# Performance work log

Hardware: AMD Instinct MI355X
Metric: run time of the kernel (lower is better)

Reference implementation:

```python
import jax, jax.numpy as jnp
import numpy as np

N = 50000        # node_num
E = 1600000      # num edges
F_IN = 8
HID = 1000
R = 100          # robustness_length


def setup_inputs() -> dict:
    key = jax.random.key(0)
    ks = jax.random.split(key, 16)
    X = jax.random.normal(ks[0], (N, F_IN), dtype=jnp.float32)
    edge_index = jax.random.randint(ks[1], (2, E), 0, N, dtype=jnp.int64)
    s = 1.0 / np.sqrt(F_IN)
    # SAGEConv mean-aggr params (PyG: out = lin_l(aggr) + lin_r(x), lin_r has no bias)
    lin_l_w = jax.random.uniform(ks[2], (1, F_IN), jnp.float32, -s, s)
    lin_l_b = jax.random.uniform(ks[3], (1,), jnp.float32, -s, s)
    lin_r_w = jax.random.uniform(ks[4], (1, F_IN), jnp.float32, -s, s)
    # SAGEConv max-aggr params
    lin_l1_w = jax.random.uniform(ks[5], (1, F_IN), jnp.float32, -s, s)
    lin_l1_b = jax.random.uniform(ks[6], (1,), jnp.float32, -s, s)
    lin_r1_w = jax.random.uniform(ks[7], (1, F_IN), jnp.float32, -s, s)
    # MLP params
    s0 = 1.0 / np.sqrt(N)
    W0 = jax.random.uniform(ks[8], (HID, N), jnp.float32, -s0, s0)
    b0 = jax.random.uniform(ks[9], (HID,), jnp.float32, -s0, s0)
    s1 = 1.0 / np.sqrt(HID)
    W1 = jax.random.uniform(ks[10], (HID, HID), jnp.float32, -s1, s1)
    b1 = jax.random.uniform(ks[11], (HID,), jnp.float32, -s1, s1)
    W2 = jax.random.uniform(ks[12], (R, HID), jnp.float32, -s1, s1)
    b2 = jax.random.uniform(ks[13], (R,), jnp.float32, -s1, s1)
    return dict(X=X, edge_index=edge_index,
                lin_l_w=lin_l_w, lin_l_b=lin_l_b, lin_r_w=lin_r_w,
                lin_l1_w=lin_l1_w, lin_l1_b=lin_l1_b, lin_r1_w=lin_r1_w,
                W0=W0, b0=b0, W1=W1, b1=b1, W2=W2, b2=b2)


def reference(X, edge_index, lin_l_w, lin_l_b, lin_r_w,
              lin_l1_w, lin_l1_b, lin_r1_w,
              W0, b0, W1, b1, W2, b2):
    src, dst = edge_index[0], edge_index[1]
    msgs = X[src]  # [E, F_IN] gathered neighbor features
    cnt = jax.ops.segment_sum(jnp.ones((E,), jnp.float32), dst, num_segments=N)
    # mean aggregation (empty -> 0)
    agg_mean = jax.ops.segment_sum(msgs, dst, num_segments=N) / jnp.maximum(cnt, 1.0)[:, None]
    # max aggregation (empty -> 0, per PyG scatter-max fill)
    agg_max = jax.ops.segment_max(msgs, dst, num_segments=N)
    agg_max = jnp.where(cnt[:, None] > 0, agg_max, 0.0)
    # SAGEConv: lin_l(aggr) + lin_r(x)
    h_mean = jax.nn.relu(agg_mean @ lin_l_w.T + lin_l_b + X @ lin_r_w.T)   # [N,1]
    h_max = jax.nn.relu(agg_max @ lin_l1_w.T + lin_l1_b + X @ lin_r1_w.T)  # [N,1]
    x = (h_mean + h_max).reshape(-1)  # [N]
    X_embedding = x
    h = jax.nn.relu(W0 @ x + b0)
    h = jax.nn.relu(W1 @ h + b1)
    out = jax.nn.relu(W2 @ h + b2)
    return (X_embedding, out)
```

## Files before the change

### kernel.cpp

```cpp
#include <hip/hip_runtime.h>

#define N_NODES 50000
#define N_EDGES 1600000
#define F_IN 8
#define HID 1000
#define R_OUT 100

#define NGRP 8
#define BSHIFT 6
#define NPB 64
#define NB 782
#define CAP_B 448
#define NCHUNK0 25


__device__ __forceinline__ unsigned fkey(float f) {
    unsigned b = __float_as_uint(f);
    return (b & 0x80000000u) ? ~b : (b | 0x80000000u);
}
__device__ __forceinline__ float funkey(unsigned k) {
    unsigned b = (k & 0x80000000u) ? (k & 0x7fffffffu) : ~k;
    return __uint_as_float(b);
}

__global__ void init_ws(unsigned* __restrict__ p, int n) {
    int i = blockIdx.x * blockDim.x + threadIdx.x;
    if (i < n) p[i] = 0u;
}

__global__ void bin_kernel(const int* __restrict__ ei,
                           const float* __restrict__ X,
                           const float* __restrict__ wl,
                           int* __restrict__ bcnt,
                           unsigned* __restrict__ binned,
                           int* __restrict__ ovf_cnt,
                           float* __restrict__ ovf_sum,
                           unsigned* __restrict__ ovf_max) {
    int e = blockIdx.x * blockDim.x + threadIdx.x;
    if (e >= N_EDGES) return;
    int src = ei[e];
    int dst = ei[N_EDGES + e];
    int b = dst >> BSHIFT;
    int g = blockIdx.x & (NGRP - 1);
    int slot = g * NB + b;
    int pos = atomicAdd(&bcnt[slot], 1);
    if (pos < CAP_B) {
        binned[(size_t)slot * CAP_B + pos] = (unsigned)src | ((unsigned)(dst & (NPB - 1)) << 16);
    } else {
        const float4* X4 = (const float4*)(X + src * F_IN);
        float4 a = X4[0], bb = X4[1];
        float f[8] = {a.x, a.y, a.z, a.w, bb.x, bb.y, bb.z, bb.w};
        float d = 0.f;
#pragma unroll
        for (int k = 0; k < 8; ++k) d += f[k] * wl[k];
        atomicAdd(&ovf_cnt[dst], 1);
        atomicAdd(&ovf_sum[dst], d);
        unsigned* mb = ovf_max + (size_t)dst * 8;
#pragma unroll
        for (int k = 0; k < 8; ++k) atomicMax(&mb[k], fkey(f[k]));
    }
}

__global__ void agg_kernel(const int* __restrict__ bcnt,
                           const unsigned* __restrict__ binned,
                           const int* __restrict__ ovf_cnt,
                           const float* __restrict__ ovf_sum,
                           const unsigned* __restrict__ ovf_max,
                           const float* __restrict__ X,
                           const float* __restrict__ lin_l_w,
                           const float* __restrict__ lin_l_b,
                           const float* __restrict__ lin_r_w,
                           const float* __restrict__ lin_l1_w,
                           const float* __restrict__ lin_l1_b,
                           const float* __restrict__ lin_r1_w,
                           float* __restrict__ xemb) {
    __shared__ unsigned lds[NPB * 10];
    float* sdot = (float*)lds;
    unsigned* scnt = lds + NPB;
    unsigned* smax = lds + 2 * NPB;

    int b = blockIdx.x;
    int tid = threadIdx.x;

    for (int i = tid; i < NPB * 10; i += 256) lds[i] = 0u;
    __syncthreads();

    float wl[8];
#pragma unroll
    for (int k = 0; k < 8; ++k) wl[k] = lin_l_w[k];

    for (int g = 0; g < NGRP; ++g) {
        int slot = g * NB + b;
        int n = bcnt[slot];
        if (n > CAP_B) n = CAP_B;
        const unsigned* list = binned + (size_t)slot * CAP_B;
        for (int j = tid; j < n; j += 256) {
            unsigned p = list[j];
            int src = p & 0xFFFF;
            int dlow = p >> 16;
            const float4* X4 = (const float4*)(X + src * F_IN);
            float4 a = X4[0], bb = X4[1];
            float f[8] = {a.x, a.y, a.z, a.w, bb.x, bb.y, bb.z, bb.w};
            float d = 0.f;
#pragma unroll
            for (int k = 0; k < 8; ++k) d += f[k] * wl[k];
            atomicAdd(&sdot[dlow], d);
            atomicAdd(&scnt[dlow], 1u);
#pragma unroll
            for (int k = 0; k < 8; ++k) atomicMax(&smax[k * NPB + dlow], fkey(f[k]));
        }
    }
    __syncthreads();

    if (tid < NPB) {
        int node = b * NPB + tid;
        if (node < N_NODES) {
            int total = (int)scnt[tid] + ovf_cnt[node];
            float sumdot = sdot[tid] + ovf_sum[node];
            float mx[8];
#pragma unroll
            for (int k = 0; k < 8; ++k) mx[k] = funkey(smax[k * NPB + tid]);
            if (ovf_cnt[node] > 0) {
                const unsigned* mb = ovf_max + (size_t)node * 8;
#pragma unroll
                for (int k = 0; k < 8; ++k) mx[k] = fmaxf(mx[k], funkey(mb[k]));
            }
            float c = (float)total;
            float mean_dot = sumdot / fmaxf(c, 1.0f);
            const float4* X4 = (const float4*)(X + node * F_IN);
            float4 a = X4[0], bb = X4[1];
            float f[8] = {a.x, a.y, a.z, a.w, bb.x, bb.y, bb.z, bb.w};
            float dr = 0.f, dr1 = 0.f, dmax = 0.f;
            bool nonempty = (total > 0);
#pragma unroll
            for (int k = 0; k < 8; ++k) {
                float m = nonempty ? mx[k] : 0.0f;
                dmax += m * lin_l1_w[k];
                dr   += f[k] * lin_r_w[k];
                dr1  += f[k] * lin_r1_w[k];
            }
            float hm = fmaxf(mean_dot + lin_l_b[0] + dr, 0.f);
            float hx = fmaxf(dmax + lin_l1_b[0] + dr1, 0.f);
            xemb[node] = hm + hx;
        }
    }
}


template <int BLOCK, int NCHUNK>
__global__ void gemv_partial(const float* __restrict__ W,
                             const float* __restrict__ x,
                             float* __restrict__ part, int cols) {
    int row = blockIdx.x;
    int c = blockIdx.y;
    int chunk = cols / NCHUNK;
    const float4* W4 = (const float4*)(W + (size_t)row * cols + (size_t)c * chunk);
    const float4* x4 = (const float4*)(x + c * chunk);
    int n4 = chunk >> 2;
    float s = 0.f;
    for (int j = threadIdx.x; j < n4; j += BLOCK) {
        float4 w = W4[j], xx = x4[j];
        s += w.x * xx.x + w.y * xx.y + w.z * xx.z + w.w * xx.w;
    }
#pragma unroll
    for (int off = 32; off > 0; off >>= 1) s += __shfl_down(s, off, 64);
    __shared__ float red[BLOCK / 64];
    int t = threadIdx.x;
    if ((t & 63) == 0) red[t >> 6] = s;
    __syncthreads();
    if (t == 0) {
        float tot = 0.f;
#pragma unroll
        for (int w = 0; w < BLOCK / 64; ++w) tot += red[w];
        part[row * NCHUNK + c] = tot;
    }
}

template <int NCHUNK>
__global__ void gemv_finalize(const float* __restrict__ part,
                              const float* __restrict__ bias,
                              float* __restrict__ y, int rows) {
    int r = blockIdx.x * blockDim.x + threadIdx.x;
    if (r >= rows) return;
    float s = 0.f;
#pragma unroll
    for (int c = 0; c < NCHUNK; ++c) s += part[r * NCHUNK + c];
    y[r] = fmaxf(s + bias[r], 0.f);
}

template <int BLOCK>
__global__ void gemv_relu(const float* __restrict__ W,
                          const float* __restrict__ x,
                          const float* __restrict__ bias,
                          float* __restrict__ y, int cols) {
    int row = blockIdx.x;
    const float4* W4 = (const float4*)(W + (size_t)row * cols);
    const float4* x4 = (const float4*)x;
    int n4 = cols >> 2;
    float s = 0.f;
    for (int j = threadIdx.x; j < n4; j += BLOCK) {
        float4 w = W4[j], xx = x4[j];
        s += w.x * xx.x + w.y * xx.y + w.z * xx.z + w.w * xx.w;
    }
#pragma unroll
    for (int off = 32; off > 0; off >>= 1) s += __shfl_down(s, off, 64);
    __shared__ float red[BLOCK / 64];
    int t = threadIdx.x;
    if ((t & 63) == 0) red[t >> 6] = s;
    __syncthreads();
    if (t == 0) {
        float tot = 0.f;
#pragma unroll
        for (int w = 0; w < BLOCK / 64; ++w) tot += red[w];
        y[row] = fmaxf(tot + bias[row], 0.f);
    }
}


__global__ void edge_kernel_fb(const int* __restrict__ ei,
                               const float* __restrict__ X,
                               const float* __restrict__ wl,
                               float* __restrict__ sumw,
                               float* __restrict__ cnt,
                               unsigned* __restrict__ maxb) {
    int e = blockIdx.x * blockDim.x + threadIdx.x;
    if (e >= N_EDGES) return;
    int src = ei[e];
    int dst = ei[N_EDGES + e];
    const float4* X4 = (const float4*)(X + src * F_IN);
    float4 a = X4[0], b = X4[1];
    float f[8] = {a.x, a.y, a.z, a.w, b.x, b.y, b.z, b.w};
    float d = 0.f;
#pragma unroll
    for (int k = 0; k < 8; ++k) d += f[k] * wl[k];
    atomicAdd(&sumw[dst], d);
    atomicAdd(&cnt[dst], 1.0f);
    unsigned* mb = maxb + (size_t)dst * 8;
#pragma unroll
    for (int k = 0; k < 8; ++k) atomicMax(&mb[k], fkey(f[k]));
}

__global__ void node_kernel_fb(const float* __restrict__ X,
                               const float* __restrict__ sumw,
                               const float* __restrict__ cnt,
                               const unsigned* __restrict__ maxb,
                               const float* __restrict__ lin_l_b,
                               const float* __restrict__ lin_r_w,
                               const float* __restrict__ lin_l1_w,
                               const float* __restrict__ lin_l1_b,
                               const float* __restrict__ lin_r1_w,
                               float* __restrict__ xout) {
    int i = blockIdx.x * blockDim.x + threadIdx.x;
    if (i >= N_NODES) return;
    float c = cnt[i];
    float mean_dot = sumw[i] / fmaxf(c, 1.0f);
    const float4* X4 = (const float4*)(X + i * F_IN);
    float4 a = X4[0], b = X4[1];
    float f[8] = {a.x, a.y, a.z, a.w, b.x, b.y, b.z, b.w};
    const uint4* M4 = (const uint4*)(maxb + (size_t)i * 8);
    uint4 m0 = M4[0], m1 = M4[1];
    unsigned mk[8] = {m0.x, m0.y, m0.z, m0.w, m1.x, m1.y, m1.z, m1.w};
    float dr = 0.f, dr1 = 0.f, dmax = 0.f;
    bool nonempty = (c > 0.f);
#pragma unroll
    for (int k = 0; k < 8; ++k) {
        float mxv = nonempty ? funkey(mk[k]) : 0.0f;
        dmax += mxv * lin_l1_w[k];
        dr   += f[k] * lin_r_w[k];
        dr1  += f[k] * lin_r1_w[k];
    }
    float hm = fmaxf(mean_dot + lin_l_b[0] + dr, 0.f);
    float hx = fmaxf(dmax + lin_l1_b[0] + dr1, 0.f);
    xout[i] = hm + hx;
}


extern "C" void kernel_launch(void* const* d_in, const int* in_sizes, int n_in,
                              void* d_out, int out_size, void* d_ws, size_t ws_size,
                              hipStream_t stream) {
    const float* X        = (const float*)d_in[0];
    const int*   ei       = (const int*)d_in[1];
    const float* lin_l_w  = (const float*)d_in[2];
    const float* lin_l_b  = (const float*)d_in[3];
    const float* lin_r_w  = (const float*)d_in[4];
    const float* lin_l1_w = (const float*)d_in[5];
    const float* lin_l1_b = (const float*)d_in[6];
    const float* lin_r1_w = (const float*)d_in[7];
    const float* W0       = (const float*)d_in[8];
    const float* b0       = (const float*)d_in[9];
    const float* W1       = (const float*)d_in[10];
    const float* b1       = (const float*)d_in[11];
    const float* W2       = (const float*)d_in[12];
    const float* b2       = (const float*)d_in[13];

    float* xemb = (float*)d_out;
    float* out2 = xemb + N_NODES;

    const size_t zero_words = (size_t)NGRP * NB + (size_t)N_NODES * 10;
    const size_t need_words = zero_words + (size_t)NGRP * NB * CAP_B
                              + (size_t)HID * NCHUNK0 + 2 * HID;
    if (ws_size >= need_words * 4) {
        int*      bcnt    = (int*)d_ws;
        int*      ovf_cnt = bcnt + NGRP * NB;
        float*    ovf_sum = (float*)(ovf_cnt + N_NODES);
        unsigned* ovf_max = (unsigned*)(ovf_sum + N_NODES);
        unsigned* binned  = ovf_max + (size_t)N_NODES * 8;
        float*    part0   = (float*)(binned + (size_t)NGRP * NB * CAP_B);
        float*    h0      = part0 + HID * NCHUNK0;
        float*    h1      = h0 + HID;

        hipLaunchKernelGGL(init_ws, dim3(((int)zero_words + 255) / 256), dim3(256), 0, stream,
                           (unsigned*)d_ws, (int)zero_words);
        hipLaunchKernelGGL(bin_kernel, dim3((N_EDGES + 255) / 256), dim3(256), 0, stream,
                           ei, X, lin_l_w, bcnt, binned, ovf_cnt, ovf_sum, ovf_max);
        hipLaunchKernelGGL(agg_kernel, dim3(NB), dim3(256), 0, stream,
                           bcnt, binned, ovf_cnt, ovf_sum, ovf_max, X,
                           lin_l_w, lin_l_b, lin_r_w, lin_l1_w, lin_l1_b, lin_r1_w, xemb);

        hipLaunchKernelGGL((gemv_partial<256, NCHUNK0>), dim3(HID, NCHUNK0), dim3(256), 0, stream,
                           W0, xemb, part0, N_NODES);
        hipLaunchKernelGGL(gemv_finalize<NCHUNK0>, dim3((HID + 255) / 256), dim3(256), 0, stream,
                           part0, b0, h0, HID);
        hipLaunchKernelGGL(gemv_relu<256>, dim3(HID), dim3(256), 0, stream,
                           W1, h0, b1, h1, HID);
        hipLaunchKernelGGL(gemv_relu<256>, dim3(R_OUT), dim3(256), 0, stream,
                           W2, h1, b2, out2, HID);
    } else {
        float*    sumw = (float*)d_ws;
        float*    cntf = sumw + N_NODES;
        unsigned* maxb = (unsigned*)(cntf + N_NODES);
        float*    h0   = (float*)(maxb + (size_t)N_NODES * 8);
        float*    h1   = h0 + HID;

        int zw = N_NODES * 10;
        hipLaunchKernelGGL(init_ws, dim3((zw + 255) / 256), dim3(256), 0, stream,
                           (unsigned*)d_ws, zw);
        hipLaunchKernelGGL(edge_kernel_fb, dim3((N_EDGES + 255) / 256), dim3(256), 0, stream,
                           ei, X, lin_l_w, sumw, cntf, maxb);
        hipLaunchKernelGGL(node_kernel_fb, dim3((N_NODES + 255) / 256), dim3(256), 0, stream,
                           X, sumw, cntf, maxb, lin_l_b, lin_r_w, lin_l1_w, lin_l1_b,
                           lin_r1_w, xemb);
        hipLaunchKernelGGL(gemv_relu<256>, dim3(HID), dim3(256), 0, stream,
                           W0, xemb, b0, h0, N_NODES);
        hipLaunchKernelGGL(gemv_relu<256>, dim3(HID), dim3(256), 0, stream,
                           W1, h0, b1, h1, HID);
        hipLaunchKernelGGL(gemv_relu<256>, dim3(R_OUT), dim3(256), 0, stream,
                           W2, h1, b2, out2, HID);
    }
}
```

Measured before the change: 426.6 us.

## Bin edges with per-block LDS histogram and one global cursor per bin

Replaces per-edge global atomics on eight grouped bin counters with a two-pass scheme. Each block of 4096 edges first builds a local histogram of destination bins in shared memory, then reserves a contiguous range per bin with a single global atomic, then scatters edges using LDS atomics. Bins become single lists of capacity 2400, so the aggregation kernel reads one list instead of eight. The cost is reading the destination indices twice and having fewer, longer-running bin blocks.

```diff
diff --git a/kernel.cpp b/kernel.cpp
--- a/kernel.cpp
+++ b/kernel.cpp
@@ -6,11 +6,12 @@
 #define HID 1000
 #define R_OUT 100
 
-#define NGRP 8
 #define BSHIFT 6
 #define NPB 64
 #define NB 782
-#define CAP_B 448
+#define CAP_B 2400
+#define CHUNK 4096
+#define NBIN_BLOCKS ((N_EDGES + CHUNK - 1) / CHUNK)
 #define NCHUNK0 25
 
 
@@ -31,37 +32,60 @@
 __global__ void bin_kernel(const int* __restrict__ ei,
                            const float* __restrict__ X,
                            const float* __restrict__ wl,
-                           int* __restrict__ bcnt,
+                           int* __restrict__ cursor,
                            unsigned* __restrict__ binned,
                            int* __restrict__ ovf_cnt,
                            float* __restrict__ ovf_sum,
                            unsigned* __restrict__ ovf_max) {
-    int e = blockIdx.x * blockDim.x + threadIdx.x;
-    if (e >= N_EDGES) return;
-    int src = ei[e];
-    int dst = ei[N_EDGES + e];
-    int b = dst >> BSHIFT;
-    int g = blockIdx.x & (NGRP - 1);
-    int slot = g * NB + b;
-    int pos = atomicAdd(&bcnt[slot], 1);
-    if (pos < CAP_B) {
-        binned[(size_t)slot * CAP_B + pos] = (unsigned)src | ((unsigned)(dst & (NPB - 1)) << 16);
-    } else {
-        const float4* X4 = (const float4*)(X + src * F_IN);
-        float4 a = X4[0], bb = X4[1];
-        float f[8] = {a.x, a.y, a.z, a.w, bb.x, bb.y, bb.z, bb.w};
-        float d = 0.f;
-#pragma unroll
-        for (int k = 0; k < 8; ++k) d += f[k] * wl[k];
-        atomicAdd(&ovf_cnt[dst], 1);
-        atomicAdd(&ovf_sum[dst], d);
-        unsigned* mb = ovf_max + (size_t)dst * 8;
-#pragma unroll
-        for (int k = 0; k < 8; ++k) atomicMax(&mb[k], fkey(f[k]));
-    }
-}
-
-__global__ void agg_kernel(const int* __restrict__ bcnt,
+    __shared__ int hist[NB];
+    __shared__ int pos[NB];
+    __shared__ int base[NB];
+    int tid = threadIdx.x;
+    int e0 = blockIdx.x * CHUNK;
+    int e1 = e0 + CHUNK;
+    if (e1 > N_EDGES) e1 = N_EDGES;
+
+    for (int i = tid; i < NB; i += 256) { hist[i] = 0; pos[i] = 0; }
+    __syncthreads();
+
+    for (int e = e0 + tid; e < e1; e += 256) {
+        int dst = ei[N_EDGES + e];
+        atomicAdd(&hist[dst >> BSHIFT], 1);
+    }
+    __syncthreads();
+
+    for (int b = tid; b < NB; b += 256) {
+        int h = hist[b];
+        base[b] = (h > 0) ? atomicAdd(&cursor[b], h) : 0;
+    }
+    __syncthreads();
+
+    for (int e = e0 + tid; e < e1; e += 256) {
+        int src = ei[e];
+        int dst = ei[N_EDGES + e];
+        int b = dst >> BSHIFT;
+        int p = atomicAdd(&pos[b], 1);
+        int gp = base[b] + p;
+        if (gp < CAP_B) {
+            binned[(size_t)b * CAP_B + gp] =
+                (unsigned)src | ((unsigned)(dst & (NPB - 1)) << 16);
+        } else {
+            const float4* X4 = (const float4*)(X + src * F_IN);
+            float4 a = X4[0], bb = X4[1];
+            float f[8] = {a.x, a.y, a.z, a.w, bb.x, bb.y, bb.z, bb.w};
+            float d = 0.f;
+#pragma unroll
+            for (int k = 0; k < 8; ++k) d += f[k] * wl[k];
+            atomicAdd(&ovf_cnt[dst], 1);
+            atomicAdd(&ovf_sum[dst], d);
+            unsigned* mb = ovf_max + (size_t)dst * 8;
+#pragma unroll
+            for (int k = 0; k < 8; ++k) atomicMax(&mb[k], fkey(f[k]));
+        }
+    }
+}
+
+__global__ void agg_kernel(const int* __restrict__ cursor,
                            const unsigned* __restrict__ binned,
                            const int* __restrict__ ovf_cnt,
                            const float* __restrict__ ovf_sum,
@@ -89,38 +113,36 @@
 #pragma unroll
     for (int k = 0; k < 8; ++k) wl[k] = lin_l_w[k];
 
-    for (int g = 0; g < NGRP; ++g) {
-        int slot = g * NB + b;
-        int n = bcnt[slot];
-        if (n > CAP_B) n = CAP_B;
-        const unsigned* list = binned + (size_t)slot * CAP_B;
-        for (int j = tid; j < n; j += 256) {
-            unsigned p = list[j];
-            int src = p & 0xFFFF;
-            int dlow = p >> 16;
-            const float4* X4 = (const float4*)(X + src * F_IN);
-            float4 a = X4[0], bb = X4[1];
-            float f[8] = {a.x, a.y, a.z, a.w, bb.x, bb.y, bb.z, bb.w};
-            float d = 0.f;
-#pragma unroll
-            for (int k = 0; k < 8; ++k) d += f[k] * wl[k];
-            atomicAdd(&sdot[dlow], d);
-            atomicAdd(&scnt[dlow], 1u);
-#pragma unroll
-            for (int k = 0; k < 8; ++k) atomicMax(&smax[k * NPB + dlow], fkey(f[k]));
-        }
+    int n = cursor[b];
+    if (n > CAP_B) n = CAP_B;
+    const unsigned* list = binned + (size_t)b * CAP_B;
+    for (int j = tid; j < n; j += 256) {
+        unsigned p = list[j];
+        int src = p & 0xFFFF;
+        int dlow = p >> 16;
+        const float4* X4 = (const float4*)(X + src * F_IN);
+        float4 a = X4[0], bb = X4[1];
+        float f[8] = {a.x, a.y, a.z, a.w, bb.x, bb.y, bb.z, bb.w};
+        float d = 0.f;
+#pragma unroll
+        for (int k = 0; k < 8; ++k) d += f[k] * wl[k];
+        atomicAdd(&sdot[dlow], d);
+        atomicAdd(&scnt[dlow], 1u);
+#pragma unroll
+        for (int k = 0; k < 8; ++k) atomicMax(&smax[k * NPB + dlow], fkey(f[k]));
     }
     __syncthreads();
 
     if (tid < NPB) {
         int node = b * NPB + tid;
         if (node < N_NODES) {
-            int total = (int)scnt[tid] + ovf_cnt[node];
+            int oc = ovf_cnt[node];
+            int total = (int)scnt[tid] + oc;
             float sumdot = sdot[tid] + ovf_sum[node];
             float mx[8];
 #pragma unroll
             for (int k = 0; k < 8; ++k) mx[k] = funkey(smax[k * NPB + tid]);
-            if (ovf_cnt[node] > 0) {
+            if (oc > 0) {
                 const unsigned* mb = ovf_max + (size_t)node * 8;
 #pragma unroll
                 for (int k = 0; k < 8; ++k) mx[k] = fmaxf(mx[k], funkey(mb[k]));
@@ -296,25 +318,25 @@
     float* xemb = (float*)d_out;
     float* out2 = xemb + N_NODES;
 
-    const size_t zero_words = (size_t)NGRP * NB + (size_t)N_NODES * 10;
-    const size_t need_words = zero_words + (size_t)NGRP * NB * CAP_B
+    const size_t zero_words = (size_t)NB + (size_t)N_NODES * 10;
+    const size_t need_words = zero_words + (size_t)NB * CAP_B
                               + (size_t)HID * NCHUNK0 + 2 * HID;
     if (ws_size >= need_words * 4) {
-        int*      bcnt    = (int*)d_ws;
-        int*      ovf_cnt = bcnt + NGRP * NB;
+        int*      cursor  = (int*)d_ws;
+        int*      ovf_cnt = cursor + NB;
         float*    ovf_sum = (float*)(ovf_cnt + N_NODES);
         unsigned* ovf_max = (unsigned*)(ovf_sum + N_NODES);
         unsigned* binned  = ovf_max + (size_t)N_NODES * 8;
-        float*    part0   = (float*)(binned + (size_t)NGRP * NB * CAP_B);
+        float*    part0   = (float*)(binned + (size_t)NB * CAP_B);
         float*    h0      = part0 + HID * NCHUNK0;
         float*    h1      = h0 + HID;
 
         hipLaunchKernelGGL(init_ws, dim3(((int)zero_words + 255) / 256), dim3(256), 0, stream,
                            (unsigned*)d_ws, (int)zero_words);
-        hipLaunchKernelGGL(bin_kernel, dim3((N_EDGES + 255) / 256), dim3(256), 0, stream,
-                           ei, X, lin_l_w, bcnt, binned, ovf_cnt, ovf_sum, ovf_max);
+        hipLaunchKernelGGL(bin_kernel, dim3(NBIN_BLOCKS), dim3(256), 0, stream,
+                           ei, X, lin_l_w, cursor, binned, ovf_cnt, ovf_sum, ovf_max);
         hipLaunchKernelGGL(agg_kernel, dim3(NB), dim3(256), 0, stream,
-                           bcnt, binned, ovf_cnt, ovf_sum, ovf_max, X,
+                           cursor, binned, ovf_cnt, ovf_sum, ovf_max, X,
                            lin_l_w, lin_l_b, lin_r_w, lin_l1_w, lin_l1_b, lin_r1_w, xemb);
 
         hipLaunchKernelGGL((gemv_partial<256, NCHUNK0>), dim3(HID, NCHUNK0), dim3(256), 0, stream,
```

Measured after the change: 380.0 us. -10.9%, faster.
